# Kernel tuning notes

Measured on AMD Instinct MI355X. Metric: run time of the kernel, lower is better.

The kernel has to match this reference:

```python
import jax, jax.numpy as jnp
import numpy as np

H = 1024
NH = 16
HD = H // NH  # 64


def setup_inputs() -> dict:
    key = jax.random.key(0)
    ks = jax.random.split(key, 7)
    s = 1.0 / np.sqrt(H)
    return {
        "hidden_states": jax.random.normal(ks[0], (4, 2048, H), dtype=jnp.float32),
        "Wq": jax.random.normal(ks[1], (H, H), dtype=jnp.float32) * s,
        "bq": jnp.zeros((H,), dtype=jnp.float32),
        "Wk": jax.random.normal(ks[2], (H, H), dtype=jnp.float32) * s,
        "bk": jnp.zeros((H,), dtype=jnp.float32),
        "Wv": jax.random.normal(ks[3], (H, H), dtype=jnp.float32) * s,
        "bv": jnp.zeros((H,), dtype=jnp.float32),
    }


def _split_heads(x):
    # [B,S,H] -> [B,NH,S,HD]
    b, s, _ = x.shape
    return x.reshape(b, s, NH, HD).transpose(0, 2, 1, 3)


def reference(hidden_states, Wq, bq, Wk, bk, Wv, bv):
    q = _split_heads(hidden_states @ Wq + bq)
    k = _split_heads(hidden_states @ Wk + bk)
    v = _split_heads(hidden_states @ Wv + bv)
    scores = jnp.einsum("bhqd,bhkd->bhqk", q, k) / jnp.sqrt(jnp.float32(HD))
    probs = jax.nn.softmax(scores, axis=-1)  # dropout p=0 (eval) -> identity
    ctx = jnp.einsum("bhqk,bhkd->bhqd", probs, v)
    b, _, s, _ = ctx.shape
    return ctx.transpose(0, 2, 1, 3).reshape(b, s, H)
```

## Files before the change

kernel.cpp:

```cpp
#include <hip/hip_runtime.h>
#include <hip/hip_bf16.h>

#define BB  4
#define SS  2048
#define HH  1024
#define NHH 16
#define HDD 64

typedef unsigned short u16;
typedef unsigned int   u32;
using bf16x8 = __attribute__((ext_vector_type(8))) short;
using f32x4  = __attribute__((ext_vector_type(4))) float;

__device__ __forceinline__ u16 f2b(float f) {
    union { float f; u32 u; } x; x.f = f;
    return (u16)((x.u + 0x7fffu + ((x.u >> 16) & 1u)) >> 16);
}
__device__ __forceinline__ u16 f2b_fast(float f) {
    union { float f; u32 u; } x; x.f = f;
    return (u16)((x.u + 0x8000u) >> 16);
}

__device__ __forceinline__ void gload16(const u16* g, u16* l) {
    __builtin_amdgcn_global_load_lds(
        (const __attribute__((address_space(1))) void*)g,
        (__attribute__((address_space(3))) void*)l, 16, 0, 0);
}

__global__ __launch_bounds__(256) void conv_x(const float* __restrict__ X,
                                              u16* __restrict__ Xb) {
    const int i = blockIdx.x * 256 + threadIdx.x;
    float4 a = ((const float4*)X)[i * 2];
    float4 b = ((const float4*)X)[i * 2 + 1];
    ushort4 s0, s1;
    s0.x = f2b(a.x); s0.y = f2b(a.y); s0.z = f2b(a.z); s0.w = f2b(a.w);
    s1.x = f2b(b.x); s1.y = f2b(b.y); s1.z = f2b(b.z); s1.w = f2b(b.w);
    ((ushort4*)Xb)[i * 2] = s0;
    ((ushort4*)Xb)[i * 2 + 1] = s1;
}

__global__ __launch_bounds__(256) void conv_wt(const float* __restrict__ Wq,
                                               const float* __restrict__ Wk,
                                               const float* __restrict__ Wv,
                                               u16* __restrict__ Wt) {
    const int z = blockIdx.z;
    const float* W = (z == 0) ? Wq : (z == 1) ? Wk : Wv;
    u16* out = Wt + (size_t)z * HH * HH;
    __shared__ float T[32][33];
    const int k0 = blockIdx.x * 32, n0 = blockIdx.y * 32;
    const int t = threadIdx.x;
    {
        const int kl = t >> 3, n4 = (t & 7) * 4;
        float4 v = *(const float4*)&W[(size_t)(k0 + kl) * HH + n0 + n4];
        T[n4 + 0][kl] = v.x; T[n4 + 1][kl] = v.y;
        T[n4 + 2][kl] = v.z; T[n4 + 3][kl] = v.w;
    }
    __syncthreads();
    {
        const int nl = t >> 3, k4 = (t & 7) * 4;
        ushort4 s;
        s.x = f2b(T[nl][k4 + 0]); s.y = f2b(T[nl][k4 + 1]);
        s.z = f2b(T[nl][k4 + 2]); s.w = f2b(T[nl][k4 + 3]);
        *(ushort4*)&out[(size_t)(n0 + nl) * HH + k0 + k4] = s;
    }
}

__global__ __launch_bounds__(256) void qkv_gemm(
    const u16* __restrict__ Xb, const u16* __restrict__ Wtb,
    const float* __restrict__ bq, const float* __restrict__ bk,
    const float* __restrict__ bv,
    u16* __restrict__ Qw, u16* __restrict__ Kw, u16* __restrict__ Vw)
{
    const int z  = blockIdx.z;
    const float* bias = (z == 0) ? bq : (z == 1) ? bk : bv;
    const int m0 = blockIdx.x * 128, n0 = blockIdx.y * 128;

    __shared__ __align__(16) u16 Xs[128 * 64];
    __shared__ __align__(16) u16 Ws[128 * 64];

    const int t = threadIdx.x;
    const int w = t >> 6, lane = t & 63, lr = lane & 15, quad = lane >> 4;
    const int l3 = lane >> 3, c7 = lane & 7;
    const int cl = (c7 ^ l3) * 8;
    const int wm = w >> 1, wn = w & 1;

    const u16* Wtz = Wtb + (size_t)z * HH * HH;

    f32x4 acc[4][4];
    #pragma unroll
    for (int i = 0; i < 4; i++)
        #pragma unroll
        for (int j = 0; j < 4; j++) acc[i][j] = f32x4{0.f, 0.f, 0.f, 0.f};

    for (int k0 = 0; k0 < HH; k0 += 64) {
        #pragma unroll
        for (int e = 0; e < 4; e++) {
            const int r = w * 32 + e * 8 + l3;
            gload16(&Xb [(size_t)(m0 + r) * HH + k0 + cl], &Xs[(w * 32 + e * 8) * 64]);
            gload16(&Wtz[(size_t)(n0 + r) * HH + k0 + cl], &Ws[(w * 32 + e * 8) * 64]);
        }
        __syncthreads();

        #pragma unroll
        for (int kc = 0; kc < 2; kc++) {
            bf16x8 af[4], bfr[4];
            const int ph = ((kc * 4 + quad) ^ c7) * 8;
            #pragma unroll
            for (int mi = 0; mi < 4; mi++)
                af[mi] = *(const bf16x8*)&Xs[(wm * 64 + mi * 16 + lr) * 64 + ph];
            #pragma unroll
            for (int ni = 0; ni < 4; ni++)
                bfr[ni] = *(const bf16x8*)&Ws[(wn * 64 + ni * 16 + lr) * 64 + ph];
            #pragma unroll
            for (int mi = 0; mi < 4; mi++)
                #pragma unroll
                for (int ni = 0; ni < 4; ni++)
                    acc[mi][ni] = __builtin_amdgcn_mfma_f32_16x16x32_bf16(
                        af[mi], bfr[ni], acc[mi][ni], 0, 0, 0);
        }
        __syncthreads();
    }

    float bvv[4];
    #pragma unroll
    for (int ni = 0; ni < 4; ni++)
        bvv[ni] = bias[n0 + wn * 64 + ni * 16 + lr];

    const float cs = (z == 0) ? 0.18033688011112042f : 1.0f;

    #pragma unroll
    for (int mi = 0; mi < 4; mi++)
        #pragma unroll
        for (int ni = 0; ni < 4; ni++) {
            const int mb = m0 + wm * 64 + mi * 16 + quad * 4;
            const int b = mb >> 11, s0 = mb & 2047;
            const int n = n0 + wn * 64 + ni * 16 + lr;
            const int h = n >> 6, d = n & 63;
            if (z == 2) {
                ushort4 vs;
                vs.x = f2b(acc[mi][ni][0] + bvv[ni]);
                vs.y = f2b(acc[mi][ni][1] + bvv[ni]);
                vs.z = f2b(acc[mi][ni][2] + bvv[ni]);
                vs.w = f2b(acc[mi][ni][3] + bvv[ni]);
                *(ushort4*)&Vw[((size_t)(b * NHH + h) * HDD + d) * SS + s0] = vs;
            } else {
                u16* dst = (z == 0) ? Qw : Kw;
                #pragma unroll
                for (int r = 0; r < 4; r++)
                    dst[((size_t)(b * NHH + h) * SS + s0 + r) * HDD + d] =
                        f2b((acc[mi][ni][r] + bvv[ni]) * cs);
            }
        }
}

__global__ __launch_bounds__(512) void attn(
    const u16* __restrict__ Qb, const u16* __restrict__ Kb,
    const u16* __restrict__ Vtb, float* __restrict__ Out)
{
    const int bid = blockIdx.x;
    const int hh = bid & 63, qt = bid >> 6;
    const int b = hh >> 4, h = hh & 15;
    const size_t hb = (size_t)hh * SS * HDD;

    __shared__ __align__(16) u16 Ks[2][64 * 64];
    __shared__ __align__(16) u16 Vs[2][64 * 64];
    __shared__ __align__(16) u16 Ps[8][16 * 72];

    const int t = threadIdx.x;
    const int w = t >> 6, lane = t & 63, lr = lane & 15, quad = lane >> 4;
    const int l3 = lane >> 3, c7 = lane & 7;
    const int cl = (c7 ^ l3) * 8;

    bf16x8 qa[2];
    #pragma unroll
    for (int kc = 0; kc < 2; kc++)
        qa[kc] = *(const bf16x8*)&Qb[hb + (size_t)(qt * 128 + w * 16 + lr) * HDD
                                     + kc * 32 + quad * 8];

    {
        const int r8 = w * 8 + l3;
        gload16(&Kb [hb + (size_t)r8 * HDD + cl], &Ks[0][w * 8 * 64]);
        gload16(&Vtb[hb + (size_t)r8 * SS + cl],  &Vs[0][w * 8 * 64]);
    }
    __syncthreads();

    float lsum[4] = {0.f, 0.f, 0.f, 0.f};
    f32x4 oc[4];
    #pragma unroll
    for (int ni = 0; ni < 4; ni++) oc[ni] = f32x4{0.f, 0.f, 0.f, 0.f};

    for (int kt = 0; kt < SS / 64; kt++) {
        const int bb = kt & 1;
        if (kt + 1 < SS / 64) {
            const int r8 = w * 8 + l3;
            gload16(&Kb [hb + (size_t)((kt + 1) * 64 + r8) * HDD + cl],
                    &Ks[bb ^ 1][w * 8 * 64]);
            gload16(&Vtb[hb + (size_t)r8 * SS + (kt + 1) * 64 + cl],
                    &Vs[bb ^ 1][w * 8 * 64]);
        }

        f32x4 sc4[4];
        #pragma unroll
        for (int ni = 0; ni < 4; ni++) sc4[ni] = f32x4{0.f, 0.f, 0.f, 0.f};
        #pragma unroll
        for (int kc = 0; kc < 2; kc++) {
            const int ph = ((kc * 4 + quad) ^ c7) * 8;
            #pragma unroll
            for (int ni = 0; ni < 4; ni++) {
                bf16x8 kf = *(const bf16x8*)&Ks[bb][(ni * 16 + lr) * 64 + ph];
                sc4[ni] = __builtin_amdgcn_mfma_f32_16x16x32_bf16(qa[kc], kf, sc4[ni], 0, 0, 0);
            }
        }

        #pragma unroll
        for (int ni = 0; ni < 4; ni++)
            #pragma unroll
            for (int r = 0; r < 4; r++) {
                const float pv = __builtin_amdgcn_exp2f(sc4[ni][r]);
                lsum[r] += pv;
                Ps[w][(quad * 4 + r) * 72 + ni * 16 + lr] = f2b_fast(pv);
            }

        bf16x8 pa[2];
        #pragma unroll
        for (int kc = 0; kc < 2; kc++)
            pa[kc] = *(const bf16x8*)&Ps[w][lr * 72 + kc * 32 + quad * 8];

        #pragma unroll
        for (int kc = 0; kc < 2; kc++) {
            const int ph = ((kc * 4 + quad) ^ c7) * 8;
            #pragma unroll
            for (int ni = 0; ni < 4; ni++) {
                bf16x8 vf = *(const bf16x8*)&Vs[bb][(ni * 16 + lr) * 64 + ph];
                oc[ni] = __builtin_amdgcn_mfma_f32_16x16x32_bf16(pa[kc], vf, oc[ni], 0, 0, 0);
            }
        }
        __syncthreads();
    }

    #pragma unroll
    for (int off = 1; off < 16; off <<= 1)
        #pragma unroll
        for (int r = 0; r < 4; r++)
            lsum[r] += __shfl_xor(lsum[r], off);

    float inv[4];
    #pragma unroll
    for (int r = 0; r < 4; r++) inv[r] = 1.0f / lsum[r];
    #pragma unroll
    for (int ni = 0; ni < 4; ni++)
        #pragma unroll
        for (int r = 0; r < 4; r++) {
            const int rq = qt * 128 + w * 16 + quad * 4 + r;
            Out[((size_t)(b * SS + rq)) * HH + h * HDD + ni * 16 + lr] =
                oc[ni][r] * inv[r];
        }
}

extern "C" void kernel_launch(void* const* d_in, const int* in_sizes, int n_in,
                              void* d_out, int out_size, void* d_ws, size_t ws_size,
                              hipStream_t stream) {
    const float* X  = (const float*)d_in[0];
    const float* Wq = (const float*)d_in[1];
    const float* bq = (const float*)d_in[2];
    const float* Wk = (const float*)d_in[3];
    const float* bk = (const float*)d_in[4];
    const float* Wv = (const float*)d_in[5];
    const float* bv = (const float*)d_in[6];
    float* Out = (float*)d_out;

    const size_t elems = (size_t)BB * SS * HH;
    u16* Qw = (u16*)d_ws;
    u16* Kw = Qw + elems;
    u16* Vw = Kw + elems;
    u16* Xb = (u16*)d_out;
    u16* Wt = Xb + elems;

    conv_x <<<dim3((int)(elems / 8 / 256)), 256, 0, stream>>>(X, Xb);
    conv_wt<<<dim3(32, 32, 3), 256, 0, stream>>>(Wq, Wk, Wv, Wt);
    qkv_gemm<<<dim3(64, 8, 3), 256, 0, stream>>>(Xb, Wt, bq, bk, bv, Qw, Kw, Vw);
    attn<<<dim3(1024), 512, 0, stream>>>(Qw, Kw, Vw, Out);
}
```

Before: 263.3 us.

## Merge conversion kernels, vectorize Q/K stores via swapped MFMA, swizzle P buffer

Merges the X and weight bf16 conversion kernels into a single launch to save one kernel launch. For the Q and K projections, the MFMA operands are swapped so each lane holds four consecutive head-dim values, which lets the epilogue write ushort4 vectors instead of scattered 2-byte stores. The attention P scratch buffer drops its padding and uses an XOR swizzle, which cuts LDS usage while aiming to avoid bank conflicts. The main risks are the extra branch in the GEMM inner loop and any mistakes in the swizzle index math.

```diff
diff --git a/kernel.cpp b/kernel.cpp
--- a/kernel.cpp
+++ b/kernel.cpp
@@ -27,28 +27,31 @@
         (__attribute__((address_space(3))) void*)l, 16, 0, 0);
 }
 
-__global__ __launch_bounds__(256) void conv_x(const float* __restrict__ X,
-                                              u16* __restrict__ Xb) {
-    const int i = blockIdx.x * 256 + threadIdx.x;
-    float4 a = ((const float4*)X)[i * 2];
-    float4 b = ((const float4*)X)[i * 2 + 1];
-    ushort4 s0, s1;
-    s0.x = f2b(a.x); s0.y = f2b(a.y); s0.z = f2b(a.z); s0.w = f2b(a.w);
-    s1.x = f2b(b.x); s1.y = f2b(b.y); s1.z = f2b(b.z); s1.w = f2b(b.w);
-    ((ushort4*)Xb)[i * 2] = s0;
-    ((ushort4*)Xb)[i * 2 + 1] = s1;
-}
-
-__global__ __launch_bounds__(256) void conv_wt(const float* __restrict__ Wq,
-                                               const float* __restrict__ Wk,
-                                               const float* __restrict__ Wv,
-                                               u16* __restrict__ Wt) {
-    const int z = blockIdx.z;
+__global__ __launch_bounds__(256) void conv(
+    const float* __restrict__ X,
+    const float* __restrict__ Wq, const float* __restrict__ Wk,
+    const float* __restrict__ Wv,
+    u16* __restrict__ Xb, u16* __restrict__ Wt)
+{
+    const int bid = blockIdx.x;
+    const int t = threadIdx.x;
+    if (bid < 4096) {
+        const int i = bid * 256 + t;
+        float4 a = ((const float4*)X)[i * 2];
+        float4 b = ((const float4*)X)[i * 2 + 1];
+        ushort4 s0, s1;
+        s0.x = f2b(a.x); s0.y = f2b(a.y); s0.z = f2b(a.z); s0.w = f2b(a.w);
+        s1.x = f2b(b.x); s1.y = f2b(b.y); s1.z = f2b(b.z); s1.w = f2b(b.w);
+        ((ushort4*)Xb)[i * 2] = s0;
+        ((ushort4*)Xb)[i * 2 + 1] = s1;
+        return;
+    }
+    const int idx = bid - 4096;
+    const int z = idx >> 10, rem = idx & 1023;
+    const int k0 = (rem >> 5) * 32, n0 = (rem & 31) * 32;
     const float* W = (z == 0) ? Wq : (z == 1) ? Wk : Wv;
     u16* out = Wt + (size_t)z * HH * HH;
     __shared__ float T[32][33];
-    const int k0 = blockIdx.x * 32, n0 = blockIdx.y * 32;
-    const int t = threadIdx.x;
     {
         const int kl = t >> 3, n4 = (t & 7) * 4;
         float4 v = *(const float4*)&W[(size_t)(k0 + kl) * HH + n0 + n4];
@@ -111,46 +114,63 @@
             #pragma unroll
             for (int ni = 0; ni < 4; ni++)
                 bfr[ni] = *(const bf16x8*)&Ws[(wn * 64 + ni * 16 + lr) * 64 + ph];
-            #pragma unroll
-            for (int mi = 0; mi < 4; mi++)
+            if (z != 2) {
                 #pragma unroll
-                for (int ni = 0; ni < 4; ni++)
-                    acc[mi][ni] = __builtin_amdgcn_mfma_f32_16x16x32_bf16(
-                        af[mi], bfr[ni], acc[mi][ni], 0, 0, 0);
+                for (int mi = 0; mi < 4; mi++)
+                    #pragma unroll
+                    for (int ni = 0; ni < 4; ni++)
+                        acc[mi][ni] = __builtin_amdgcn_mfma_f32_16x16x32_bf16(
+                            bfr[ni], af[mi], acc[mi][ni], 0, 0, 0);
+            } else {
+                #pragma unroll
+                for (int mi = 0; mi < 4; mi++)
+                    #pragma unroll
+                    for (int ni = 0; ni < 4; ni++)
+                        acc[mi][ni] = __builtin_amdgcn_mfma_f32_16x16x32_bf16(
+                            af[mi], bfr[ni], acc[mi][ni], 0, 0, 0);
+            }
         }
         __syncthreads();
     }
 
-    float bvv[4];
-    #pragma unroll
-    for (int ni = 0; ni < 4; ni++)
-        bvv[ni] = bias[n0 + wn * 64 + ni * 16 + lr];
-
-    const float cs = (z == 0) ? 0.18033688011112042f : 1.0f;
-
-    #pragma unroll
-    for (int mi = 0; mi < 4; mi++)
-        #pragma unroll
-        for (int ni = 0; ni < 4; ni++) {
-            const int mb = m0 + wm * 64 + mi * 16 + quad * 4;
-            const int b = mb >> 11, s0 = mb & 2047;
-            const int n = n0 + wn * 64 + ni * 16 + lr;
-            const int h = n >> 6, d = n & 63;
-            if (z == 2) {
+    if (z != 2) {
+        u16* dst = (z == 0) ? Qw : Kw;
+        const float cs = (z == 0) ? 0.18033688011112042f : 1.0f;
+        #pragma unroll
+        for (int mi = 0; mi < 4; mi++) {
+            const int sg = m0 + wm * 64 + mi * 16 + lr;
+            const int b = sg >> 11, s = sg & 2047;
+            #pragma unroll
+            for (int ni = 0; ni < 4; ni++) {
+                const int nb = n0 + wn * 64 + ni * 16 + quad * 4;
+                const int h = nb >> 6, d0 = nb & 63;
+                float4 bb4 = *(const float4*)&bias[nb];
                 ushort4 vs;
-                vs.x = f2b(acc[mi][ni][0] + bvv[ni]);
-                vs.y = f2b(acc[mi][ni][1] + bvv[ni]);
-                vs.z = f2b(acc[mi][ni][2] + bvv[ni]);
-                vs.w = f2b(acc[mi][ni][3] + bvv[ni]);
+                vs.x = f2b((acc[mi][ni][0] + bb4.x) * cs);
+                vs.y = f2b((acc[mi][ni][1] + bb4.y) * cs);
+                vs.z = f2b((acc[mi][ni][2] + bb4.z) * cs);
+                vs.w = f2b((acc[mi][ni][3] + bb4.w) * cs);
+                *(ushort4*)&dst[((size_t)(b * NHH + h) * SS + s) * HDD + d0] = vs;
+            }
+        }
+    } else {
+        #pragma unroll
+        for (int mi = 0; mi < 4; mi++)
+            #pragma unroll
+            for (int ni = 0; ni < 4; ni++) {
+                const int mb = m0 + wm * 64 + mi * 16 + quad * 4;
+                const int b = mb >> 11, s0 = mb & 2047;
+                const int n = n0 + wn * 64 + ni * 16 + lr;
+                const int h = n >> 6, d = n & 63;
+                const float bv4 = bias[n];
+                ushort4 vs;
+                vs.x = f2b(acc[mi][ni][0] + bv4);
+                vs.y = f2b(acc[mi][ni][1] + bv4);
+                vs.z = f2b(acc[mi][ni][2] + bv4);
+                vs.w = f2b(acc[mi][ni][3] + bv4);
                 *(ushort4*)&Vw[((size_t)(b * NHH + h) * HDD + d) * SS + s0] = vs;
-            } else {
-                u16* dst = (z == 0) ? Qw : Kw;
-                #pragma unroll
-                for (int r = 0; r < 4; r++)
-                    dst[((size_t)(b * NHH + h) * SS + s0 + r) * HDD + d] =
-                        f2b((acc[mi][ni][r] + bvv[ni]) * cs);
-            }
-        }
+            }
+    }
 }
 
 __global__ __launch_bounds__(512) void attn(
@@ -164,7 +184,7 @@
 
     __shared__ __align__(16) u16 Ks[2][64 * 64];
     __shared__ __align__(16) u16 Vs[2][64 * 64];
-    __shared__ __align__(16) u16 Ps[8][16 * 72];
+    __shared__ __align__(16) u16 Ps[8][16 * 64];
 
     const int t = threadIdx.x;
     const int w = t >> 6, lane = t & 63, lr = lane & 15, quad = lane >> 4;
@@ -218,13 +238,15 @@
             for (int r = 0; r < 4; r++) {
                 const float pv = __builtin_amdgcn_exp2f(sc4[ni][r]);
                 lsum[r] += pv;
-                Ps[w][(quad * 4 + r) * 72 + ni * 16 + lr] = f2b_fast(pv);
+                const int row = quad * 4 + r;
+                const int pc = ((ni * 2 + (lr >> 3)) ^ (row & 7)) * 8 + (lr & 7);
+                Ps[w][row * 64 + pc] = f2b_fast(pv);
             }
 
         bf16x8 pa[2];
         #pragma unroll
         for (int kc = 0; kc < 2; kc++)
-            pa[kc] = *(const bf16x8*)&Ps[w][lr * 72 + kc * 32 + quad * 8];
+            pa[kc] = *(const bf16x8*)&Ps[w][lr * 64 + (((kc * 4 + quad) ^ (lr & 7)) * 8)];
 
         #pragma unroll
         for (int kc = 0; kc < 2; kc++) {
@@ -276,8 +298,7 @@
     u16* Xb = (u16*)d_out;
     u16* Wt = Xb + elems;
 
-    conv_x <<<dim3((int)(elems / 8 / 256)), 256, 0, stream>>>(X, Xb);
-    conv_wt<<<dim3(32, 32, 3), 256, 0, stream>>>(Wq, Wk, Wv, Wt);
+    conv<<<dim3(4096 + 3072), 256, 0, stream>>>(X, Wq, Wk, Wv, Xb, Wt);
     qkv_gemm<<<dim3(64, 8, 3), 256, 0, stream>>>(Xb, Wt, bq, bk, bv, Qw, Kw, Vw);
     attn<<<dim3(1024), 512, 0, stream>>>(Qw, Kw, Vw, Out);
 }
```

Measured after the change: 280.1 us. +6.4%, slower.
